# Kernel optimization log

Measured on AMD Instinct MI355X. Metric: run time of the kernel, lower is better.

The kernel has to match this reference:

```python
import jax, jax.numpy as jnp
import numpy as np
from jax import lax

K = 8  # window / output_stride (hardcoded in original forward)
BN_EPS = 1e-5


def setup_inputs() -> dict:
    key = jax.random.key(0)
    ks = jax.random.split(key, 4)
    B, C, H, W = 4, 56, 320, 320
    return {
        "x": jax.random.normal(ks[0], (B, C, H, W), jnp.float32),
        "conv1_w": jax.random.normal(ks[1], (56, 56), jnp.float32) * 0.01,
        "conv1_b": jnp.zeros((56,), jnp.float32),
        "conv2_w": jax.random.normal(ks[2], (1, 56), jnp.float32) * 0.01,
        "conv2_b": jnp.zeros((1,), jnp.float32),
        "bn1_gamma": jnp.ones((56,), jnp.float32),
        "bn1_beta": jnp.zeros((56,), jnp.float32),
        "bn2_gamma": jnp.ones((1,), jnp.float32),
        "bn2_beta": jnp.zeros((1,), jnp.float32),
    }


def _batchnorm(y, gamma, beta):
    # training-mode BatchNorm2d: stats over (N, H, W) per channel
    mean = jnp.mean(y, axis=(0, 2, 3), keepdims=True)
    var = jnp.var(y, axis=(0, 2, 3), keepdims=True)
    yhat = (y - mean) * lax.rsqrt(var + BN_EPS)
    return yhat * gamma[None, :, None, None] + beta[None, :, None, None]


def _counter(x, w1, b1, w2, b2, g1, be1, g2, be2):
    # AvgPool2d(kernel=8, stride=1) -> [B,56,H-7,W-7]
    p = lax.reduce_window(x, 0.0, lax.add, (1, 1, K, K), (1, 1, 1, 1), "VALID") / (K * K)
    y = jnp.einsum("oc,bchw->bohw", w1, p) + b1[None, :, None, None]
    y = jax.nn.relu(_batchnorm(y, g1, be1))
    y = jnp.einsum("oc,bchw->bohw", w2, y) + b2[None, :, None, None]
    y = jax.nn.relu(_batchnorm(y, g2, be2))
    return y  # [B,1,Hc,Wc]


def _dynamic_unfolding(x, local_count):
    # x: [B,C,H,W], local_count: [B,1,H-7,W-7]
    B, C, H, W = x.shape
    Hc, Wc = H - K + 1, W - K + 1
    m = jnp.mean(x, axis=1)  # [B,H,W]
    # extract all 8x8 sliding windows -> [B,Hc,Wc,64]
    patches = jnp.stack(
        [m[:, di:di + Hc, dj:dj + Wc] for di in range(K) for dj in range(K)],
        axis=-1,
    )
    sm = jax.nn.softmax(patches, axis=-1)  # per-window softmax
    wgt = sm * local_count[:, 0, :, :, None]  # [B,Hc,Wc,64]
    # overlapping fold (scatter-add) back to [B,1,H,W]
    R = jnp.zeros((B, H, W), x.dtype)
    for di in range(K):
        for dj in range(K):
            R = R.at[:, di:di + Hc, dj:dj + Wc].add(wgt[..., di * K + dj])
    return R[:, None, :, :]


def reference(x, conv1_w, conv1_b, conv2_w, conv2_b, bn1_gamma, bn1_beta, bn2_gamma, bn2_beta):
    C_out = _counter(x, conv1_w, conv1_b, conv2_w, conv2_b, bn1_gamma, bn1_beta, bn2_gamma, bn2_beta)
    R = _dynamic_unfolding(x, C_out)
    return C_out, R
```

## Files before the change

kernel.cpp:

```cpp
#include <hip/hip_runtime.h>
#include <math.h>

#define B 4
#define C 56
#define H 320
#define W 320
#define HC 313
#define WC 313
#define NIMG (H*W)
#define NSP  (HC*WC)
#define NPIX (B*NSP)
#define NM   (B*NIMG)
#define BN_EPS 1e-5f
#define NGRID 512

#define PHR 39
#define NF4 390

typedef __attribute__((ext_vector_type(8))) short short8;
typedef __attribute__((ext_vector_type(16))) float float16;
typedef __attribute__((ext_vector_type(4))) float f32x4;

__device__ __forceinline__ unsigned short f2bf(float v) {
  unsigned int u = __float_as_uint(v);
  return (unsigned short)((u + 0x7fffu + ((u >> 16) & 1u)) >> 16);
}

__global__ __launch_bounds__(256) void pool32_kernel(
    const float* __restrict__ x, float* __restrict__ Epart,
    unsigned short* __restrict__ p_t) {
  __shared__ float tin[PHR][40];
  __shared__ float hs[PHR][33];
  __shared__ unsigned short Pt[8][1024];
  const int tid = threadIdx.x;
  int bid = blockIdx.x;
  const int g = bid % 7; bid /= 7;
  const int b = bid & 3; bid >>= 2;
  const int ty = bid / 10, tx = bid - (bid / 10) * 10;
  const int i0 = ty * 32, j0 = tx * 32;
  const float* xg = x + ((size_t)b * C + g * 8) * NIMG;

  int r4[2], q4[2]; bool act[2], vld[2], inter[2]; size_t xoff[2];
  #pragma unroll
  for (int k = 0; k < 2; ++k) {
    int idx = tid + k * 256;
    r4[k] = idx / 10; q4[k] = idx - r4[k] * 10;
    act[k] = idx < NF4;
    vld[k] = act[k] && (i0 + r4[k] < H) && (j0 + q4[k] * 4 < W);
    inter[k] = act[k] && r4[k] < 32 && q4[k] < 8;
    xoff[k] = (size_t)(i0 + r4[k]) * W + j0 + q4[k] * 4;
  }
  f32x4 cur4[2], nxt4[2];
  #pragma unroll
  for (int k = 0; k < 2; ++k)
    cur4[k] = vld[k] ? *(const f32x4*)(xg + xoff[k]) : (f32x4){0.f, 0.f, 0.f, 0.f};

  f32x4 esum4[2] = {{0.f, 0.f, 0.f, 0.f}, {0.f, 0.f, 0.f, 0.f}};

  const int vs = tid >> 5, vj = tid & 31;

  #pragma unroll
  for (int c = 0; c < 8; ++c) {
    #pragma unroll
    for (int k = 0; k < 2; ++k) {
      if (act[k]) *(f32x4*)&tin[r4[k]][q4[k] * 4] = cur4[k];
      if (inter[k]) esum4[k] += cur4[k];
    }
    __syncthreads();
    if (c < 7) {
      const float* xp = xg + (size_t)(c + 1) * NIMG;
      #pragma unroll
      for (int k = 0; k < 2; ++k)
        nxt4[k] = vld[k] ? *(const f32x4*)(xp + xoff[k]) : (f32x4){0.f, 0.f, 0.f, 0.f};
    }
    #pragma unroll
    for (int t = tid; t < PHR * 8; t += 256) {
      int r = t >> 3, c0 = (t & 7) * 4;
      float v[11];
      #pragma unroll
      for (int d = 0; d < 11; ++d) v[d] = tin[r][c0 + d];
      float s0 = ((v[0] + v[1]) + (v[2] + v[3])) + ((v[4] + v[5]) + (v[6] + v[7]));
      float s1 = s0 - v[0] + v[8];
      float s2 = s1 - v[1] + v[9];
      float s3 = s2 - v[2] + v[10];
      hs[r][c0] = s0; hs[r][c0 + 1] = s1; hs[r][c0 + 2] = s2; hs[r][c0 + 3] = s3;
    }
    __syncthreads();
    {
      float w[11];
      int ib = vs * 4;
      #pragma unroll
      for (int d = 0; d < 11; ++d) w[d] = hs[ib + d][vj];
      float t0 = ((w[0] + w[1]) + (w[2] + w[3])) + ((w[4] + w[5]) + (w[6] + w[7]));
      float t1 = t0 - w[0] + w[8];
      float t2 = t1 - w[1] + w[9];
      float t3 = t2 - w[2] + w[10];
      Pt[c][(ib + 0) * 32 + vj] = f2bf(t0 * (1.f / 64.f));
      Pt[c][(ib + 1) * 32 + vj] = f2bf(t1 * (1.f / 64.f));
      Pt[c][(ib + 2) * 32 + vj] = f2bf(t2 * (1.f / 64.f));
      Pt[c][(ib + 3) * 32 + vj] = f2bf(t3 * (1.f / 64.f));
    }
    #pragma unroll
    for (int k = 0; k < 2; ++k) cur4[k] = nxt4[k];
  }
  __syncthreads();

  float* Eb = Epart + ((size_t)g * B + b) * NIMG;
  #pragma unroll
  for (int k = 0; k < 2; ++k)
    if (inter[k]) *(f32x4*)&Eb[(i0 + r4[k]) * W + j0 + q4[k] * 4] = esum4[k];

  unsigned short* pg = p_t + (size_t)g * NPIX * 8;
  #pragma unroll
  for (int k = 0; k < 4; ++k) {
    int idx = tid + k * 256;
    int i = idx >> 5, j = idx & 31;
    int gi = i0 + i, gj = j0 + j;
    if (gi < HC && gj < WC) {
      unsigned short t8[8];
      #pragma unroll
      for (int c2 = 0; c2 < 8; ++c2) t8[c2] = Pt[c2][idx];
      *(short8*)(pg + ((size_t)b * NSP + gi * WC + gj) * 8) = *(short8*)t8;
    }
  }
}

__global__ __launch_bounds__(256) void se_pool_kernel(
    const float* __restrict__ Epart, float* __restrict__ E, float* __restrict__ S) {
  __shared__ float tin[39][40];
  __shared__ float hs[39][33];
  const int b = blockIdx.z;
  const int i0 = blockIdx.y * 32, j0 = blockIdx.x * 32;
  const int tid = threadIdx.x;
  for (int idx = tid; idx < 39 * 39; idx += 256) {
    int r = idx / 39, cc = idx - r * 39;
    int gi = i0 + r, gj = j0 + cc;
    float v = 0.f;
    if (gi < H && gj < W) {
      float s = 0.f;
      #pragma unroll
      for (int g = 0; g < 7; ++g)
        s += Epart[((size_t)g * B + b) * NIMG + gi * W + gj];
      v = expf(s * (1.f / C));
      if (r < 32 && cc < 32) E[(size_t)b * NIMG + gi * W + gj] = v;
    }
    tin[r][cc] = v;
  }
  __syncthreads();
  for (int idx = tid; idx < 39 * 32; idx += 256) {
    int r = idx >> 5, j = idx & 31;
    float s = 0.f;
    #pragma unroll
    for (int d = 0; d < 8; ++d) s += tin[r][j + d];
    hs[r][j] = s;
  }
  __syncthreads();
  for (int idx = tid; idx < 32 * 32; idx += 256) {
    int i = idx >> 5, j = idx & 31;
    int gi = i0 + i, gj = j0 + j;
    if (gi < HC && gj < WC) {
      float s = 0.f;
      #pragma unroll
      for (int d = 0; d < 8; ++d) s += hs[i + d][j];
      S[(size_t)b * NSP + gi * WC + gj] = s;
    }
  }
}

__global__ __launch_bounds__(256) void y1_stats_kernel(
    const unsigned short* __restrict__ p_t, const float* __restrict__ w1,
    float* __restrict__ ypart) {
  __shared__ unsigned short Wl[64 * 64];
  __shared__ float red[4][32][64];
  const int tid = threadIdx.x, wave = tid >> 6, lane = tid & 63;
  for (int idx = tid; idx < 4096; idx += 256) {
    int o = idx >> 6, k = idx & 63;
    float v = (o < C && k < C) ? w1[o * C + k] : 0.f;
    *(unsigned short*)((char*)Wl + (o * 128 + ((2 * k) ^ ((o & 7) << 4)))) = f2bf(v);
  }
  __syncthreads();
  short8 afr[2][4];
  #pragma unroll
  for (int q = 0; q < 2; ++q)
    #pragma unroll
    for (int ks = 0; ks < 4; ++ks) {
      int row = q * 32 + (lane & 31), kb = ks * 16 + 8 * (lane >> 5);
      afr[q][ks] = *(const short8*)((const char*)Wl + row * 128 + ((2 * kb) ^ ((row & 7) << 4)));
    }
  float s1[2][16], s2[2][16];
  #pragma unroll
  for (int q = 0; q < 2; ++q)
    #pragma unroll
    for (int r = 0; r < 16; ++r) { s1[q][r] = 0.f; s2[q][r] = 0.f; }

  const int h = lane >> 5;
  const int nchunk = (NPIX + 127) / 128;
  auto loadch = [&](int cc, short8* dst) {
    int col = cc * 128 + wave * 32 + (lane & 31);
    bool cv = (cc < nchunk) && (col < NPIX);
    size_t pofs = (size_t)(cv ? col : 0) * 8;
    #pragma unroll
    for (int ks = 0; ks < 4; ++ks) {
      int gg = ks * 2 + h;
      short8 bv = (short8){0, 0, 0, 0, 0, 0, 0, 0};
      if (gg < 7 && cv) bv = *(const short8*)(p_t + (size_t)gg * NPIX * 8 + pofs);
      dst[ks] = bv;
    }
  };
  short8 bfr[4];
  loadch(blockIdx.x, bfr);
  for (int ch = blockIdx.x; ch < nchunk; ch += NGRID) {
    short8 nbfr[4];
    loadch(ch + NGRID, nbfr);
    float16 a0 = {}, a1 = {};
    #pragma unroll
    for (int ks = 0; ks < 4; ++ks) {
      a0 = __builtin_amdgcn_mfma_f32_32x32x16_bf16(afr[0][ks], bfr[ks], a0, 0, 0, 0);
      a1 = __builtin_amdgcn_mfma_f32_32x32x16_bf16(afr[1][ks], bfr[ks], a1, 0, 0, 0);
    }
    #pragma unroll
    for (int r = 0; r < 16; ++r) {
      s1[0][r] += a0[r]; s2[0][r] = fmaf(a0[r], a0[r], s2[0][r]);
      s1[1][r] += a1[r]; s2[1][r] = fmaf(a1[r], a1[r], s2[1][r]);
    }
    #pragma unroll
    for (int ks = 0; ks < 4; ++ks) bfr[ks] = nbfr[ks];
  }
  for (int pass = 0; pass < 2; ++pass) {
    __syncthreads();
    #pragma unroll
    for (int q = 0; q < 2; ++q)
      #pragma unroll
      for (int r = 0; r < 16; ++r)
        red[wave][q * 16 + r][lane] = pass ? s2[q][r] : s1[q][r];
    __syncthreads();
    if (tid < C) {
      int row = tid, q = row >> 5, rr = row & 31;
      int hh = (rr >> 2) & 1, reg = (rr & 3) | ((rr >> 3) << 2);
      float s = 0.f;
      #pragma unroll
      for (int w = 0; w < 4; ++w)
        #pragma unroll
        for (int cl = 0; cl < 32; ++cl)
          s += red[w][q * 16 + reg][32 * hh + cl];
      ypart[blockIdx.x * 112 + pass * 56 + row] = s;
    }
  }
}

__global__ void ypart_bn1_kernel(const float* __restrict__ ypart,
                                 const float* __restrict__ g1, const float* __restrict__ be1,
                                 float* __restrict__ ac) {
  __shared__ float sums[112];
  int t = threadIdx.x;
  if (t < 112) {
    float s0 = 0.f, s1 = 0.f, s2 = 0.f, s3 = 0.f;
    #pragma unroll 4
    for (int b = 0; b < NGRID; b += 4) {
      s0 += ypart[(b + 0) * 112 + t];
      s1 += ypart[(b + 1) * 112 + t];
      s2 += ypart[(b + 2) * 112 + t];
      s3 += ypart[(b + 3) * 112 + t];
    }
    sums[t] = (s0 + s1) + (s2 + s3);
  }
  __syncthreads();
  if (t < C) {
    float m = sums[t] * (1.f / NPIX);
    float var = sums[56 + t] * (1.f / NPIX) - m * m;
    float a = g1[t] * rsqrtf(var + BN_EPS);
    ac[t] = a;
    ac[C + t] = fmaf(-a, m, be1[t]);
  }
}

__global__ __launch_bounds__(256) void y2_kernel(
    const unsigned short* __restrict__ p_t, const float* __restrict__ w1,
    const float* __restrict__ ac, const float* __restrict__ w2,
    float* __restrict__ y2, float* __restrict__ y2part) {
  __shared__ unsigned short Wl[64 * 64];
  __shared__ float af[64], cf[64], wf[64];
  const int tid = threadIdx.x, wave = tid >> 6, lane = tid & 63;
  for (int idx = tid; idx < 4096; idx += 256) {
    int o = idx >> 6, k = idx & 63;
    float v = (o < C && k < C) ? w1[o * C + k] : 0.f;
    *(unsigned short*)((char*)Wl + (o * 128 + ((2 * k) ^ ((o & 7) << 4)))) = f2bf(v);
  }
  if (tid < 64) {
    bool ok = tid < C;
    af[tid] = ok ? ac[tid] : 0.f;
    cf[tid] = ok ? ac[C + tid] : 0.f;
    wf[tid] = ok ? w2[tid] : 0.f;
  }
  __syncthreads();
  short8 afr[2][4];
  #pragma unroll
  for (int q = 0; q < 2; ++q)
    #pragma unroll
    for (int ks = 0; ks < 4; ++ks) {
      int row = q * 32 + (lane & 31), kb = ks * 16 + 8 * (lane >> 5);
      afr[q][ks] = *(const short8*)((const char*)Wl + row * 128 + ((2 * kb) ^ ((row & 7) << 4)));
    }
  const int h = lane >> 5;
  float ss1 = 0.f, ss2 = 0.f;
  const int nchunk = (NPIX + 127) / 128;
  auto loadch = [&](int cc, short8* dst) {
    int col = cc * 128 + wave * 32 + (lane & 31);
    bool cv = (cc < nchunk) && (col < NPIX);
    size_t pofs = (size_t)(cv ? col : 0) * 8;
    #pragma unroll
    for (int ks = 0; ks < 4; ++ks) {
      int gg = ks * 2 + h;
      short8 bv = (short8){0, 0, 0, 0, 0, 0, 0, 0};
      if (gg < 7 && cv) bv = *(const short8*)(p_t + (size_t)gg * NPIX * 8 + pofs);
      dst[ks] = bv;
    }
  };
  short8 bfr[4];
  loadch(blockIdx.x, bfr);
  for (int ch = blockIdx.x; ch < nchunk; ch += NGRID) {
    short8 nbfr[4];
    loadch(ch + NGRID, nbfr);
    float16 a0 = {}, a1 = {};
    #pragma unroll
    for (int ks = 0; ks < 4; ++ks) {
      a0 = __builtin_amdgcn_mfma_f32_32x32x16_bf16(afr[0][ks], bfr[ks], a0, 0, 0, 0);
      a1 = __builtin_amdgcn_mfma_f32_32x32x16_bf16(afr[1][ks], bfr[ks], a1, 0, 0, 0);
    }
    float ysum = 0.f;
    #pragma unroll
    for (int r = 0; r < 16; ++r) {
      int o0 = (r & 3) + 8 * (r >> 2) + 4 * h;
      ysum = fmaf(wf[o0], fmaxf(fmaf(af[o0], a0[r], cf[o0]), 0.f), ysum);
      int o1 = o0 + 32;
      ysum = fmaf(wf[o1], fmaxf(fmaf(af[o1], a1[r], cf[o1]), 0.f), ysum);
    }
    ysum += __shfl_xor(ysum, 32);
    int col = ch * 128 + wave * 32 + (lane & 31);
    bool wr = (col < NPIX) && lane < 32;
    if (wr) {
      y2[col] = ysum;
      ss1 += ysum;
      ss2 = fmaf(ysum, ysum, ss2);
    }
    #pragma unroll
    for (int ks = 0; ks < 4; ++ks) bfr[ks] = nbfr[ks];
  }
  #pragma unroll
  for (int off = 1; off < 64; off <<= 1) {
    ss1 += __shfl_xor(ss1, off);
    ss2 += __shfl_xor(ss2, off);
  }
  if (lane == 0) {
    y2part[(blockIdx.x * 4 + wave) * 2 + 0] = ss1;
    y2part[(blockIdx.x * 4 + wave) * 2 + 1] = ss2;
  }
}

__global__ void bn2_final_kernel(const float* __restrict__ y2part,
                                 const float* __restrict__ g2, const float* __restrict__ be2,
                                 float* __restrict__ a2c2) {
  __shared__ float red[8];
  int t = threadIdx.x;
  float s1 = 0.f, s2 = 0.f;
  for (int i = t; i < NGRID * 4; i += 256) {
    s1 += y2part[i * 2 + 0];
    s2 += y2part[i * 2 + 1];
  }
  #pragma unroll
  for (int off = 32; off > 0; off >>= 1) {
    s1 += __shfl_down(s1, off);
    s2 += __shfl_down(s2, off);
  }
  int wave = t >> 6, lane = t & 63;
  if (lane == 0) { red[wave * 2] = s1; red[wave * 2 + 1] = s2; }
  __syncthreads();
  if (t == 0) {
    s1 = red[0] + red[2] + red[4] + red[6];
    s2 = red[1] + red[3] + red[5] + red[7];
    float mean = s1 * (1.f / NPIX);
    float var  = s2 * (1.f / NPIX) - mean * mean;
    float a = g2[0] * rsqrtf(var + BN_EPS);
    a2c2[0] = a;
    a2c2[1] = fmaf(-a, mean, be2[0]);
  }
}

__global__ __launch_bounds__(256) void r_pool_kernel(
    const float* __restrict__ y2, const float* __restrict__ S,
    const float* __restrict__ a2c2, const float* __restrict__ E,
    float* __restrict__ cout, float* __restrict__ R) {
  __shared__ float tin[39][40];
  __shared__ float hs[39][33];
  const int b = blockIdx.z;
  const int i0 = blockIdx.y * 32, j0 = blockIdx.x * 32;
  const int tid = threadIdx.x;
  const float a2 = a2c2[0], c2 = a2c2[1];
  const float* y2b = y2 + (size_t)b * NSP;
  const float* Sb  = S + (size_t)b * NSP;
  float* cb = cout + (size_t)b * NSP;
  for (int idx = tid; idx < 39 * 39; idx += 256) {
    int r = idx / 39, cc = idx - r * 39;
    int gi = i0 + r - 7, gj = j0 + cc - 7;
    float t = 0.f;
    if (gi >= 0 && gi < HC && gj >= 0 && gj < WC) {
      float v = fmaxf(fmaf(a2, y2b[gi * WC + gj], c2), 0.f);
      t = v / Sb[gi * WC + gj];
      if (r >= 7 && cc >= 7) cb[gi * WC + gj] = v;
    }
    tin[r][cc] = t;
  }
  __syncthreads();
  for (int idx = tid; idx < 39 * 32; idx += 256) {
    int r = idx >> 5, j = idx & 31;
    float s = 0.f;
    #pragma unroll
    for (int d = 0; d < 8; ++d) s += tin[r][j + d];
    hs[r][j] = s;
  }
  __syncthreads();
  for (int idx = tid; idx < 32 * 32; idx += 256) {
    int i = idx >> 5, j = idx & 31;
    size_t gofs = (size_t)b * NIMG + (i0 + i) * W + (j0 + j);
    float s = 0.f;
    #pragma unroll
    for (int d = 0; d < 8; ++d) s += hs[i + d][j];
    R[gofs] = E[gofs] * s;
  }
}

extern "C" void kernel_launch(void* const* d_in, const int* in_sizes, int n_in,
                              void* d_out, int out_size, void* d_ws, size_t ws_size,
                              hipStream_t stream) {
  const float* x   = (const float*)d_in[0];
  const float* w1  = (const float*)d_in[1];
  const float* w2  = (const float*)d_in[3];
  const float* g1  = (const float*)d_in[5];
  const float* be1 = (const float*)d_in[6];
  const float* g2  = (const float*)d_in[7];
  const float* be2 = (const float*)d_in[8];

  float* out_c = (float*)d_out;
  float* out_r = out_c + NPIX;

  unsigned short* p_t = (unsigned short*)d_ws;
  float* fbase = (float*)(p_t + (size_t)7 * NPIX * 8);
  size_t off = 0;
  float* Epart  = fbase + off; off += (size_t)7 * NM;
  float* E      = fbase + off; off += NM;
  float* Sarr   = fbase + off; off += NPIX;
  float* y2     = fbase + off; off += NPIX;
  float* ypart  = fbase + off; off += (size_t)NGRID * 112;
  float* y2part = fbase + off; off += (size_t)NGRID * 8;
  float* ac     = fbase + off; off += 112;
  float* a2c2   = fbase + off; off += 2;

  pool32_kernel<<<100 * B * 7, 256, 0, stream>>>(x, Epart, p_t);

  dim3 sg(10, 10, B);
  se_pool_kernel<<<sg, 256, 0, stream>>>(Epart, E, Sarr);

  y1_stats_kernel<<<NGRID, 256, 0, stream>>>(p_t, w1, ypart);
  ypart_bn1_kernel<<<1, 128, 0, stream>>>(ypart, g1, be1, ac);
  y2_kernel<<<NGRID, 256, 0, stream>>>(p_t, w1, ac, w2, y2, y2part);
  bn2_final_kernel<<<1, 256, 0, stream>>>(y2part, g2, be2, a2c2);

  dim3 rg(10, 10, B);
  r_pool_kernel<<<rg, 256, 0, stream>>>(y2, Sarr, a2c2, E, out_c, out_r);
}
```

Measured before the change: 104.9 us.

## Deepen MFMA operand prefetch to two chunks and simplify box-sum pooling

The two MFMA GEMM kernels now keep three register buffers and prefetch two chunks ahead, which gives more time to hide global-load latency on the pooled bf16 operands. The pooling kernel's separable 8x8 box sum drops the sliding-window form (four outputs per thread) and has each thread sum 8 values directly for one output. The hs tile padding goes from 33 to 32 columns. The changes trade extra register pressure and extra LDS reads and adds for simpler indexing and more parallel work per pass.

```diff
diff --git a/kernel.cpp b/kernel.cpp
--- a/kernel.cpp
+++ b/kernel.cpp
@@ -30,7 +30,7 @@
     const float* __restrict__ x, float* __restrict__ Epart,
     unsigned short* __restrict__ p_t) {
   __shared__ float tin[PHR][40];
-  __shared__ float hs[PHR][33];
+  __shared__ float hs[PHR][32];
   __shared__ unsigned short Pt[8][1024];
   const int tid = threadIdx.x;
   int bid = blockIdx.x;
@@ -57,8 +57,6 @@
 
   f32x4 esum4[2] = {{0.f, 0.f, 0.f, 0.f}, {0.f, 0.f, 0.f, 0.f}};
 
-  const int vs = tid >> 5, vj = tid & 31;
-
   #pragma unroll
   for (int c = 0; c < 8; ++c) {
     #pragma unroll
@@ -74,31 +72,25 @@
         nxt4[k] = vld[k] ? *(const f32x4*)(xp + xoff[k]) : (f32x4){0.f, 0.f, 0.f, 0.f};
     }
     #pragma unroll
-    for (int t = tid; t < PHR * 8; t += 256) {
-      int r = t >> 3, c0 = (t & 7) * 4;
-      float v[11];
-      #pragma unroll
-      for (int d = 0; d < 11; ++d) v[d] = tin[r][c0 + d];
-      float s0 = ((v[0] + v[1]) + (v[2] + v[3])) + ((v[4] + v[5]) + (v[6] + v[7]));
-      float s1 = s0 - v[0] + v[8];
-      float s2 = s1 - v[1] + v[9];
-      float s3 = s2 - v[2] + v[10];
-      hs[r][c0] = s0; hs[r][c0 + 1] = s1; hs[r][c0 + 2] = s2; hs[r][c0 + 3] = s3;
+    for (int it = 0; it < 5; ++it) {
+      int idx = tid + it * 256;
+      if (idx < PHR * 32) {
+        int r = idx >> 5, j = idx & 31;
+        float s = 0.f;
+        #pragma unroll
+        for (int d = 0; d < 8; ++d) s += tin[r][j + d];
+        hs[r][j] = s;
+      }
     }
     __syncthreads();
-    {
-      float w[11];
-      int ib = vs * 4;
-      #pragma unroll
-      for (int d = 0; d < 11; ++d) w[d] = hs[ib + d][vj];
-      float t0 = ((w[0] + w[1]) + (w[2] + w[3])) + ((w[4] + w[5]) + (w[6] + w[7]));
-      float t1 = t0 - w[0] + w[8];
-      float t2 = t1 - w[1] + w[9];
-      float t3 = t2 - w[2] + w[10];
-      Pt[c][(ib + 0) * 32 + vj] = f2bf(t0 * (1.f / 64.f));
-      Pt[c][(ib + 1) * 32 + vj] = f2bf(t1 * (1.f / 64.f));
-      Pt[c][(ib + 2) * 32 + vj] = f2bf(t2 * (1.f / 64.f));
-      Pt[c][(ib + 3) * 32 + vj] = f2bf(t3 * (1.f / 64.f));
+    #pragma unroll
+    for (int it = 0; it < 4; ++it) {
+      int idx = tid + it * 256;
+      int i = idx >> 5, j = idx & 31;
+      float s = 0.f;
+      #pragma unroll
+      for (int d = 0; d < 8; ++d) s += hs[i + d][j];
+      Pt[c][idx] = f2bf(s * (1.f / 64.f));
     }
     #pragma unroll
     for (int k = 0; k < 2; ++k) cur4[k] = nxt4[k];
@@ -207,16 +199,16 @@
       dst[ks] = bv;
     }
   };
-  short8 bfr[4];
-  loadch(blockIdx.x, bfr);
+  short8 b0[4], b1[4], b2[4];
+  loadch(blockIdx.x, b0);
+  loadch(blockIdx.x + NGRID, b1);
   for (int ch = blockIdx.x; ch < nchunk; ch += NGRID) {
-    short8 nbfr[4];
-    loadch(ch + NGRID, nbfr);
+    loadch(ch + 2 * NGRID, b2);
     float16 a0 = {}, a1 = {};
     #pragma unroll
     for (int ks = 0; ks < 4; ++ks) {
-      a0 = __builtin_amdgcn_mfma_f32_32x32x16_bf16(afr[0][ks], bfr[ks], a0, 0, 0, 0);
-      a1 = __builtin_amdgcn_mfma_f32_32x32x16_bf16(afr[1][ks], bfr[ks], a1, 0, 0, 0);
+      a0 = __builtin_amdgcn_mfma_f32_32x32x16_bf16(afr[0][ks], b0[ks], a0, 0, 0, 0);
+      a1 = __builtin_amdgcn_mfma_f32_32x32x16_bf16(afr[1][ks], b0[ks], a1, 0, 0, 0);
     }
     #pragma unroll
     for (int r = 0; r < 16; ++r) {
@@ -224,7 +216,7 @@
       s1[1][r] += a1[r]; s2[1][r] = fmaf(a1[r], a1[r], s2[1][r]);
     }
     #pragma unroll
-    for (int ks = 0; ks < 4; ++ks) bfr[ks] = nbfr[ks];
+    for (int ks = 0; ks < 4; ++ks) { b0[ks] = b1[ks]; b1[ks] = b2[ks]; }
   }
   for (int pass = 0; pass < 2; ++pass) {
     __syncthreads();
@@ -316,16 +308,16 @@
       dst[ks] = bv;
     }
   };
-  short8 bfr[4];
-  loadch(blockIdx.x, bfr);
+  short8 b0[4], b1[4], b2[4];
+  loadch(blockIdx.x, b0);
+  loadch(blockIdx.x + NGRID, b1);
   for (int ch = blockIdx.x; ch < nchunk; ch += NGRID) {
-    short8 nbfr[4];
-    loadch(ch + NGRID, nbfr);
+    loadch(ch + 2 * NGRID, b2);
     float16 a0 = {}, a1 = {};
     #pragma unroll
     for (int ks = 0; ks < 4; ++ks) {
-      a0 = __builtin_amdgcn_mfma_f32_32x32x16_bf16(afr[0][ks], bfr[ks], a0, 0, 0, 0);
-      a1 = __builtin_amdgcn_mfma_f32_32x32x16_bf16(afr[1][ks], bfr[ks], a1, 0, 0, 0);
+      a0 = __builtin_amdgcn_mfma_f32_32x32x16_bf16(afr[0][ks], b0[ks], a0, 0, 0, 0);
+      a1 = __builtin_amdgcn_mfma_f32_32x32x16_bf16(afr[1][ks], b0[ks], a1, 0, 0, 0);
     }
     float ysum = 0.f;
     #pragma unroll
@@ -344,7 +336,7 @@
       ss2 = fmaf(ysum, ysum, ss2);
     }
     #pragma unroll
-    for (int ks = 0; ks < 4; ++ks) bfr[ks] = nbfr[ks];
+    for (int ks = 0; ks < 4; ++ks) { b0[ks] = b1[ks]; b1[ks] = b2[ks]; }
   }
   #pragma unroll
   for (int off = 1; off < 64; off <<= 1) {
```

Result: slower. 108.4 us (+3.3%).
